# Optimization experiments

Hardware: AMD Instinct MI355X
Metric: run time of the kernel (lower is better)

The kernel has to match this reference:

```python
import jax, jax.numpy as jnp
import numpy as np

B, N, D, H = 8, 1024, 512, 512  # batch, nodes/graph, input dim, hidden/output dim
NEG_SLOPE = 0.2


def _gatv2_layer(x, src, dst, Wl, bl, Wr, br, a, bias, nseg):
    """PyG GATv2Conv (heads=1, add_self_loops=False, eval mode -> no dropout).
    message j->i: alpha_ij = softmax_i( a . leaky_relu(xl[j] + xr[i]) ); out[i] = sum_j alpha_ij * xl[j] + bias
    """
    xl = x @ Wl + bl              # [nseg, H] source transform
    xr = x @ Wr + br              # [nseg, H] target transform
    e = jax.nn.leaky_relu(xl[src] + xr[dst], NEG_SLOPE) @ a  # [E] raw scores
    m = jax.lax.stop_gradient(jax.ops.segment_max(e, dst, num_segments=nseg))
    ex = jnp.exp(e - m[dst])
    s = jax.ops.segment_sum(ex, dst, num_segments=nseg)
    alpha = ex / s[dst]                                       # segment softmax over incoming edges
    out = jax.ops.segment_sum(alpha[:, None] * xl[src], dst, num_segments=nseg)
    return out + bias


def setup_inputs() -> dict:
    key = jax.random.key(0)
    rng = np.random.RandomState(0)
    # random per-graph adjacency, avg degree ~16; block-diagonal edge extraction
    adj_np = (rng.rand(B, N, N) < (16.0 / N))
    srcs, dsts = [], []
    for b in range(B):  # matches torch.nonzero(big_adj).t(): row=src, col=dst
        r, c = np.nonzero(adj_np[b])
        srcs.append(r + b * N)
        dsts.append(c + b * N)
    edge_index = jnp.asarray(np.stack([np.concatenate(srcs), np.concatenate(dsts)]).astype(np.int32))

    ks = jax.random.split(key, 32)
    def lin(k, fi, fo):
        return (jax.random.normal(k, (fi, fo), jnp.float32) / np.sqrt(fi)).astype(jnp.float32)
    inp = {
        "batch_graph": jax.random.normal(ks[0], (B, N, D), jnp.float32),
        "adj": jnp.asarray(adj_np.astype(np.float32)),
        "edge_index": edge_index,
    }
    dims = [(D, H), (H, H), (H, H)]
    for i, (fi, fo) in enumerate(dims, start=1):
        k = jax.random.split(ks[i], 6)
        inp[f"Wl{i}"] = lin(k[0], fi, fo)
        inp[f"bl{i}"] = jnp.zeros((fo,), jnp.float32)
        inp[f"Wr{i}"] = lin(k[1], fi, fo)
        inp[f"br{i}"] = jnp.zeros((fo,), jnp.float32)
        inp[f"a{i}"] = (jax.random.normal(k[2], (fo,), jnp.float32) / np.sqrt(fo)).astype(jnp.float32)
        inp[f"bias{i}"] = jnp.zeros((fo,), jnp.float32)
    return inp


def reference(batch_graph, adj, edge_index,
              Wl1, bl1, Wr1, br1, a1, bias1,
              Wl2, bl2, Wr2, br2, a2, bias2,
              Wl3, bl3, Wr3, br3, a3, bias3):
    b, n, d = batch_graph.shape
    nseg = b * n
    x = batch_graph.reshape(nseg, d)
    src, dst = edge_index[0], edge_index[1]
    x = _gatv2_layer(x, src, dst, Wl1, bl1, Wr1, br1, a1, bias1, nseg)  # graph_norm = Identity
    x = _gatv2_layer(x, src, dst, Wl2, bl2, Wr2, br2, a2, bias2, nseg)
    x = _gatv2_layer(x, src, dst, Wl3, bl3, Wr3, br3, a3, bias3, nseg)
    return x.reshape(b, n, -1)
```

## Files before the change

### kernel.cpp

```cpp
#include <hip/hip_runtime.h>
#include <math.h>

#define MTOT 8192
#define HD   512

typedef __attribute__((ext_vector_type(8))) short bf16x8;
typedef __attribute__((ext_vector_type(4))) float floatx4;

__device__ inline unsigned short f2bf(float f) {
    unsigned int u = __float_as_uint(f);
    unsigned int r = (u + 0x7FFFu + ((u >> 16) & 1u)) >> 16;
    return (unsigned short)r;
}
__device__ inline float bf2f(unsigned short h) {
    return __uint_as_float(((unsigned int)h) << 16);
}


__global__ void count_deg(const int* __restrict__ dst, int* __restrict__ deg, int E) {
    int i = blockIdx.x * 256 + threadIdx.x;
    if (i < E) atomicAdd(&deg[dst[i]], 1);
}

__global__ __launch_bounds__(1024) void scan_offsets(const int* __restrict__ deg,
                                                     int* __restrict__ offs,
                                                     int* __restrict__ cursor) {
    __shared__ int part[1024];
    int tid = threadIdx.x;
    int base = tid * 8;
    int v[8]; int s = 0;
    #pragma unroll
    for (int i = 0; i < 8; ++i) { v[i] = deg[base + i]; s += v[i]; }
    part[tid] = s;
    __syncthreads();
    for (int off = 1; off < 1024; off <<= 1) {
        int t = (tid >= off) ? part[tid - off] : 0;
        __syncthreads();
        part[tid] += t;
        __syncthreads();
    }
    int run = (tid == 0) ? 0 : part[tid - 1];
    #pragma unroll
    for (int i = 0; i < 8; ++i) {
        offs[base + i] = run;
        cursor[base + i] = run;
        run += v[i];
    }
    if (tid == 1023) offs[MTOT] = run;
}

__global__ void scatter_edges(const int* __restrict__ src, const int* __restrict__ dst,
                              int* __restrict__ cursor, int* __restrict__ csr_src, int E) {
    int i = blockIdx.x * 256 + threadIdx.x;
    if (i < E) {
        int p = atomicAdd(&cursor[dst[i]], 1);
        csr_src[p] = src[i];
    }
}


__global__ __launch_bounds__(256) void prep_convert(
    const float* __restrict__ W0, const float* __restrict__ W1,
    const float* __restrict__ W2, const float* __restrict__ W3,
    const float* __restrict__ W4, const float* __restrict__ W5,
    unsigned short* __restrict__ wtbase,
    const float* __restrict__ X,
    unsigned short* __restrict__ Ahi, unsigned short* __restrict__ Alo,
    int* __restrict__ deg)
{
    int z = blockIdx.z;
    if (z == 7) {
        if (blockIdx.x == 0 && blockIdx.y == 0)
            for (int i = threadIdx.x; i < MTOT; i += 256) deg[i] = 0;
        return;
    }
    if (z == 6) {
        int bid = blockIdx.x * 16 + blockIdx.y;
        int t0 = bid * 256 + threadIdx.x;
        #pragma unroll
        for (int it = 0; it < 16; ++it) {
            int i = (t0 + it * 65536) * 4;
            float4 vv = *(const float4*)(X + i);
            ushort4 h, l;
            h.x = f2bf(vv.x); l.x = f2bf(vv.x - bf2f(h.x));
            h.y = f2bf(vv.y); l.y = f2bf(vv.y - bf2f(h.y));
            h.z = f2bf(vv.z); l.z = f2bf(vv.z - bf2f(h.z));
            h.w = f2bf(vv.w); l.w = f2bf(vv.w - bf2f(h.w));
            *(ushort4*)(Ahi + i) = h;
            *(ushort4*)(Alo + i) = l;
        }
        return;
    }
    const float* W = (z == 0) ? W0 : (z == 1) ? W1 : (z == 2) ? W2
                   : (z == 3) ? W3 : (z == 4) ? W4 : W5;
    int L = z >> 1, lr = z & 1;
    const size_t SZ = (size_t)HD * HD;
    unsigned short* Whi = wtbase + (L * 4 + lr * 2) * SZ;
    unsigned short* Wlo = Whi + SZ;

    __shared__ float t[32][33];
    int bx = blockIdx.x * 32;
    int by = blockIdx.y * 32;
    int tx = threadIdx.x & 31, ty = threadIdx.x >> 5;
    for (int i = ty; i < 32; i += 8)
        t[i][tx] = W[(size_t)(by + i) * HD + bx + tx];
    __syncthreads();
    for (int i = ty; i < 32; i += 8) {
        float vv = t[tx][i];
        unsigned short h = f2bf(vv);
        unsigned short l = f2bf(vv - bf2f(h));
        Whi[(size_t)(bx + i) * HD + by + tx] = h;
        Wlo[(size_t)(bx + i) * HD + by + tx] = l;
    }
}


__global__ __launch_bounds__(256) void gemm_mfma_dual(
    const unsigned short* __restrict__ Ahi, const unsigned short* __restrict__ Alo,
    const unsigned short* __restrict__ Bhi_l, const unsigned short* __restrict__ Blo_l,
    const unsigned short* __restrict__ Bhi_r, const unsigned short* __restrict__ Blo_r,
    const float* __restrict__ bias_l, const float* __restrict__ bias_r,
    float* __restrict__ Cl, float* __restrict__ Cr)
{
    const unsigned short* Bhi = blockIdx.z ? Bhi_r : Bhi_l;
    const unsigned short* Blo = blockIdx.z ? Blo_r : Blo_l;
    const float* bias         = blockIdx.z ? bias_r : bias_l;
    float* C                  = blockIdx.z ? Cr : Cl;

    __shared__ __align__(16) unsigned short lds[4 * 128 * 32];

    int tid = threadIdx.x;
    int wave = tid >> 6, lane = tid & 63;
    int bm = blockIdx.y * 128, bn = blockIdx.x * 128;

    const unsigned short* gsrc[4] = {Ahi, Alo, Bhi, Blo};
    int rowbase[4] = {bm, bm, bn, bn};

    const unsigned short* gbase =
        gsrc[wave] + (size_t)(rowbase[wave] + (lane >> 2)) * 512 + (lane & 3) * 8;

    floatx4 acc[4][4] = {};

    int wm = wave & 1, wn = wave >> 1;
    int lr = lane & 15, lq = lane >> 4;

    for (int k0 = 0; k0 < 512; k0 += 32) {
        const unsigned short* g = gbase + k0;
        #pragma unroll
        for (int rg = 0; rg < 8; ++rg) {
            __builtin_amdgcn_global_load_lds(
                (const __attribute__((address_space(1))) unsigned int*)(g + (size_t)rg * 16 * 512),
                (__attribute__((address_space(3))) unsigned int*)(&lds[wave * 4096 + rg * 512]),
                16, 0, 0);
        }
        __syncthreads();

        bf16x8 ah[4], al[4], bh[4], bl_[4];
        #pragma unroll
        for (int i = 0; i < 4; ++i) {
            int mrow = wm * 64 + i * 16 + lr;
            ah[i]  = *(const bf16x8*)&lds[0 * 4096 + mrow * 32 + lq * 8];
            al[i]  = *(const bf16x8*)&lds[1 * 4096 + mrow * 32 + lq * 8];
            int nrow = wn * 64 + i * 16 + lr;
            bh[i]  = *(const bf16x8*)&lds[2 * 4096 + nrow * 32 + lq * 8];
            bl_[i] = *(const bf16x8*)&lds[3 * 4096 + nrow * 32 + lq * 8];
        }
        #pragma unroll
        for (int i = 0; i < 4; ++i)
            #pragma unroll
            for (int j = 0; j < 4; ++j) {
                acc[i][j] = __builtin_amdgcn_mfma_f32_16x16x32_bf16(ah[i], bh[j],  acc[i][j], 0, 0, 0);
                acc[i][j] = __builtin_amdgcn_mfma_f32_16x16x32_bf16(ah[i], bl_[j], acc[i][j], 0, 0, 0);
                acc[i][j] = __builtin_amdgcn_mfma_f32_16x16x32_bf16(al[i], bh[j],  acc[i][j], 0, 0, 0);
            }
        __syncthreads();
    }

    #pragma unroll
    for (int j = 0; j < 4; ++j) {
        int n = bn + wn * 64 + j * 16 + lr;
        float bv = bias[n];
        #pragma unroll
        for (int i = 0; i < 4; ++i) {
            int mbase = bm + wm * 64 + i * 16 + lq * 4;
            #pragma unroll
            for (int r = 0; r < 4; ++r)
                C[(size_t)(mbase + r) * 512 + n] = acc[i][j][r] + bv;
        }
    }
}


__global__ __launch_bounds__(512) void gat_fused3(
    const float* __restrict__ xl, const float* __restrict__ xr,
    const float* __restrict__ avec, const float* __restrict__ bias,
    const int* __restrict__ offs, const int* __restrict__ csr_src,
    float* __restrict__ out, unsigned short* __restrict__ Ohi,
    unsigned short* __restrict__ Olo, int write_fp32)
{
    __shared__ float xr_sh[4][512];
    __shared__ float sc_sh[4][128];
    __shared__ int   idx_sh[4][128];
    __shared__ float inv_sh[4];

    int gid = blockIdx.x;
    int nbase = ((gid & 7) << 10) + ((gid >> 3) << 2);
    int tid = threadIdx.x;
    int wv = tid >> 6, lane = tid & 63;

    int o0 = offs[nbase], o1 = offs[nbase + 1], o2 = offs[nbase + 2];
    int o3 = offs[nbase + 3], o4 = offs[nbase + 4];

    {
        int row = tid >> 7, col = tid & 127;
        *(float4*)&xr_sh[row][col * 4] =
            *(const float4*)(xr + (size_t)(nbase + row) * HD + col * 4);
    }
    if (wv < 4) {
        int nb = (wv == 0) ? o0 : (wv == 1) ? o1 : (wv == 2) ? o2 : o3;
        int ne = (wv == 0) ? o1 : (wv == 1) ? o2 : (wv == 2) ? o3 : o4;
        int dg = ne - nb; if (dg > 128) dg = 128;
        for (int i = lane; i < dg; i += 64) idx_sh[wv][i] = csr_src[nb + i];
    }
    __syncthreads();

    {
        int sub = lane >> 4, flane = lane & 15;
        float4 av[8];
        #pragma unroll
        for (int i = 0; i < 8; ++i)
            av[i] = *(const float4*)(avec + i * 64 + flane * 4);

        for (int p0 = o0 + wv * 4; p0 < o4; p0 += 32) {
            int p = p0 + sub;
            bool valid = p < o4;
            int pc = valid ? p : o0;
            int nid = (pc >= o1) + (pc >= o2) + (pc >= o3);
            int nb = (nid == 0) ? o0 : (nid == 1) ? o1 : (nid == 2) ? o2 : o3;
            int local = pc - nb;
            valid = valid && (local < 128);
            int j = idx_sh[nid][valid ? local : 0];
            const float* xls = xl + (size_t)j * HD;
            float pe0 = 0.f, pe1 = 0.f;
            #pragma unroll
            for (int i = 0; i < 8; ++i) {
                float4 xv = *(const float4*)(xls + i * 64 + flane * 4);
                float4 rv = *(const float4*)&xr_sh[nid][i * 64 + flane * 4];
                float t;
                t = xv.x + rv.x; pe0 = fmaf(av[i].x, t, pe0); pe1 = fmaf(av[i].x, fabsf(t), pe1);
                t = xv.y + rv.y; pe0 = fmaf(av[i].y, t, pe0); pe1 = fmaf(av[i].y, fabsf(t), pe1);
                t = xv.z + rv.z; pe0 = fmaf(av[i].z, t, pe0); pe1 = fmaf(av[i].z, fabsf(t), pe1);
                t = xv.w + rv.w; pe0 = fmaf(av[i].w, t, pe0); pe1 = fmaf(av[i].w, fabsf(t), pe1);
            }
            float pe = fmaf(0.6f, pe0, 0.4f * pe1);
            pe += __shfl_xor(pe, 1, 64);
            pe += __shfl_xor(pe, 2, 64);
            pe += __shfl_xor(pe, 4, 64);
            pe += __shfl_xor(pe, 8, 64);
            if (valid && flane == 0) sc_sh[nid][local] = pe;
        }
    }
    __syncthreads();

    if (wv < 4) {
        int nb = (wv == 0) ? o0 : (wv == 1) ? o1 : (wv == 2) ? o2 : o3;
        int ne = (wv == 0) ? o1 : (wv == 1) ? o2 : (wv == 2) ? o3 : o4;
        int dg = ne - nb; if (dg > 128) dg = 128;
        float s0v = (lane < dg) ? sc_sh[wv][lane] : -1e30f;
        float s1v = (lane + 64 < dg) ? sc_sh[wv][lane + 64] : -1e30f;
        float m = fmaxf(s0v, s1v);
        #pragma unroll
        for (int off = 32; off; off >>= 1) m = fmaxf(m, __shfl_xor(m, off, 64));
        float e0 = (lane < dg) ? __expf(s0v - m) : 0.f;
        float e1 = (lane + 64 < dg) ? __expf(s1v - m) : 0.f;
        if (lane < dg) sc_sh[wv][lane] = e0;
        if (lane + 64 < dg) sc_sh[wv][lane + 64] = e1;
        float s = e0 + e1;
        #pragma unroll
        for (int off = 32; off; off >>= 1) s += __shfl_xor(s, off, 64);
        if (lane == 0) inv_sh[wv] = (s > 0.f) ? 1.f / s : 0.f;
    }
    __syncthreads();

    int nid = wv & 3, half = wv >> 2;
    int node = nbase + nid;
    int nb = (nid == 0) ? o0 : (nid == 1) ? o1 : (nid == 2) ? o2 : o3;
    int ne = (nid == 0) ? o1 : (nid == 1) ? o2 : (nid == 2) ? o3 : o4;
    int dg = ne - nb; if (dg > 128) dg = 128;
    int hb = half * 256 + lane * 4;

    float4 acc = {0.f, 0.f, 0.f, 0.f};
    int p = 0;
    for (; p + 8 <= dg; p += 8) {
        float w[8]; const float* q[8];
        #pragma unroll
        for (int u = 0; u < 8; ++u) {
            w[u] = sc_sh[nid][p + u];
            q[u] = xl + (size_t)idx_sh[nid][p + u] * HD + hb;
        }
        float4 x[8];
        #pragma unroll
        for (int u = 0; u < 8; ++u) x[u] = *(const float4*)q[u];
        #pragma unroll
        for (int u = 0; u < 8; ++u) {
            acc.x += w[u] * x[u].x; acc.y += w[u] * x[u].y;
            acc.z += w[u] * x[u].z; acc.w += w[u] * x[u].w;
        }
    }
    for (; p < dg; ++p) {
        float w = sc_sh[nid][p];
        const float* q = xl + (size_t)idx_sh[nid][p] * HD + hb;
        float4 x = *(const float4*)q;
        acc.x += w * x.x; acc.y += w * x.y; acc.z += w * x.z; acc.w += w * x.w;
    }

    float inv = inv_sh[nid];
    float4 bv = *(const float4*)(bias + hb);
    float4 o = {acc.x * inv + bv.x, acc.y * inv + bv.y,
                acc.z * inv + bv.z, acc.w * inv + bv.w};

    if (write_fp32) {
        *(float4*)(out + (size_t)node * HD + hb) = o;
    } else {
        size_t rb = (size_t)node * HD + hb;
        ushort4 h, lo;
        h.x = f2bf(o.x); lo.x = f2bf(o.x - bf2f(h.x));
        h.y = f2bf(o.y); lo.y = f2bf(o.y - bf2f(h.y));
        h.z = f2bf(o.z); lo.z = f2bf(o.z - bf2f(h.z));
        h.w = f2bf(o.w); lo.w = f2bf(o.w - bf2f(h.w));
        *(ushort4*)(Ohi + rb) = h;
        *(ushort4*)(Olo + rb) = lo;
    }
}


extern "C" void kernel_launch(void* const* d_in, const int* in_sizes, int n_in,
                              void* d_out, int out_size, void* d_ws, size_t ws_size,
                              hipStream_t stream) {
    const float* x0 = (const float*)d_in[0];
    const int* eidx = (const int*)d_in[2];
    int E = in_sizes[2] / 2;
    const int* esrc = eidx;
    const int* edst = eidx + E;

    const float* Wl[3] = {(const float*)d_in[3],  (const float*)d_in[9],  (const float*)d_in[15]};
    const float* bl[3] = {(const float*)d_in[4],  (const float*)d_in[10], (const float*)d_in[16]};
    const float* Wr[3] = {(const float*)d_in[5],  (const float*)d_in[11], (const float*)d_in[17]};
    const float* br[3] = {(const float*)d_in[6],  (const float*)d_in[12], (const float*)d_in[18]};
    const float* av[3] = {(const float*)d_in[7],  (const float*)d_in[13], (const float*)d_in[19]};
    const float* bs[3] = {(const float*)d_in[8],  (const float*)d_in[14], (const float*)d_in[20]};

    char* w = (char*)d_ws;
    unsigned short* Ahi = (unsigned short*)w; w += (size_t)MTOT * HD * 2;
    unsigned short* Alo = (unsigned short*)w; w += (size_t)MTOT * HD * 2;
    unsigned short* wtbase = (unsigned short*)w; w += 12 * (size_t)HD * HD * 2;
    float* xl = (float*)w; w += (size_t)MTOT * HD * 4;
    float* xr = (float*)w; w += (size_t)MTOT * HD * 4;
    int* deg    = (int*)w;
    int* offs   = deg + MTOT;
    int* cursor = offs + MTOT + 8;
    int* csr    = cursor + MTOT;
    const size_t SZ = (size_t)HD * HD;

    prep_convert<<<dim3(16, 16, 8), 256, 0, stream>>>(
        Wl[0], Wr[0], Wl[1], Wr[1], Wl[2], Wr[2], wtbase, x0, Ahi, Alo, deg);
    count_deg<<<(E + 255) / 256, 256, 0, stream>>>(edst, deg, E);
    scan_offsets<<<1, 1024, 0, stream>>>(deg, offs, cursor);
    scatter_edges<<<(E + 255) / 256, 256, 0, stream>>>(esrc, edst, cursor, csr, E);

    dim3 ggrid(HD / 128, MTOT / 128, 2);
    for (int L = 0; L < 3; ++L) {
        gemm_mfma_dual<<<ggrid, 256, 0, stream>>>(Ahi, Alo,
            wtbase + (L * 4 + 0) * SZ, wtbase + (L * 4 + 1) * SZ,
            wtbase + (L * 4 + 2) * SZ, wtbase + (L * 4 + 3) * SZ,
            bl[L], br[L], xl, xr);
        int last = (L == 2);
        gat_fused3<<<MTOT / 4, 512, 0, stream>>>(xl, xr, av[L], bs[L], offs, csr,
                                                 last ? (float*)d_out : nullptr,
                                                 last ? nullptr : Ahi,
                                                 last ? nullptr : Alo,
                                                 last);
    }
}
```

Baseline: 336.1 us.

## Fold degree counting and prefix scan into prep and first GEMM launches

Removes the standalone count_deg and scan_offsets kernels. Degree counting now runs in the z==7 slice of prep_convert after a memset, and the CSR offset scan runs in an extra z==2 slice of the first dual GEMM. This cuts kernel launches and serial gaps in the CSR build, and scatter_edges now runs between the first GEMM and the first attention kernel. The trade-off is an extra memset launch and a 256-thread scan running alongside the GEMM blocks, plus a mostly idle z==2 grid slice in layer one.

```diff
diff --git a/kernel.cpp b/kernel.cpp
--- a/kernel.cpp
+++ b/kernel.cpp
@@ -17,37 +17,6 @@
 }
 
 
-__global__ void count_deg(const int* __restrict__ dst, int* __restrict__ deg, int E) {
-    int i = blockIdx.x * 256 + threadIdx.x;
-    if (i < E) atomicAdd(&deg[dst[i]], 1);
-}
-
-__global__ __launch_bounds__(1024) void scan_offsets(const int* __restrict__ deg,
-                                                     int* __restrict__ offs,
-                                                     int* __restrict__ cursor) {
-    __shared__ int part[1024];
-    int tid = threadIdx.x;
-    int base = tid * 8;
-    int v[8]; int s = 0;
-    #pragma unroll
-    for (int i = 0; i < 8; ++i) { v[i] = deg[base + i]; s += v[i]; }
-    part[tid] = s;
-    __syncthreads();
-    for (int off = 1; off < 1024; off <<= 1) {
-        int t = (tid >= off) ? part[tid - off] : 0;
-        __syncthreads();
-        part[tid] += t;
-        __syncthreads();
-    }
-    int run = (tid == 0) ? 0 : part[tid - 1];
-    #pragma unroll
-    for (int i = 0; i < 8; ++i) {
-        offs[base + i] = run;
-        cursor[base + i] = run;
-        run += v[i];
-    }
-    if (tid == 1023) offs[MTOT] = run;
-}
 
 __global__ void scatter_edges(const int* __restrict__ src, const int* __restrict__ dst,
                               int* __restrict__ cursor, int* __restrict__ csr_src, int E) {
@@ -66,12 +35,12 @@
     unsigned short* __restrict__ wtbase,
     const float* __restrict__ X,
     unsigned short* __restrict__ Ahi, unsigned short* __restrict__ Alo,
-    int* __restrict__ deg)
+    const int* __restrict__ edst, int E, int* __restrict__ deg)
 {
     int z = blockIdx.z;
     if (z == 7) {
-        if (blockIdx.x == 0 && blockIdx.y == 0)
-            for (int i = threadIdx.x; i < MTOT; i += 256) deg[i] = 0;
+        int t0 = (blockIdx.x * 16 + blockIdx.y) * 256 + threadIdx.x;
+        for (int i = t0; i < E; i += 65536) atomicAdd(&deg[edst[i]], 1);
         return;
     }
     if (z == 6) {
@@ -120,8 +89,38 @@
     const unsigned short* __restrict__ Bhi_l, const unsigned short* __restrict__ Blo_l,
     const unsigned short* __restrict__ Bhi_r, const unsigned short* __restrict__ Blo_r,
     const float* __restrict__ bias_l, const float* __restrict__ bias_r,
-    float* __restrict__ Cl, float* __restrict__ Cr)
+    float* __restrict__ Cl, float* __restrict__ Cr,
+    int do_scan, const int* __restrict__ deg,
+    int* __restrict__ offs, int* __restrict__ cursor)
 {
+    if (blockIdx.z == 2) {
+        if (do_scan && blockIdx.x == 0 && blockIdx.y == 0) {
+            __shared__ int part[256];
+            int tid = threadIdx.x;
+            int base = tid * 32;
+            int v[32]; int s = 0;
+            #pragma unroll
+            for (int i = 0; i < 32; ++i) { v[i] = deg[base + i]; s += v[i]; }
+            part[tid] = s;
+            __syncthreads();
+            for (int off = 1; off < 256; off <<= 1) {
+                int t = (tid >= off) ? part[tid - off] : 0;
+                __syncthreads();
+                part[tid] += t;
+                __syncthreads();
+            }
+            int run = tid ? part[tid - 1] : 0;
+            #pragma unroll
+            for (int i = 0; i < 32; ++i) {
+                offs[base + i] = run;
+                cursor[base + i] = run;
+                run += v[i];
+            }
+            if (tid == 255) offs[MTOT] = run;
+        }
+        return;
+    }
+
     const unsigned short* Bhi = blockIdx.z ? Bhi_r : Bhi_l;
     const unsigned short* Blo = blockIdx.z ? Blo_r : Blo_l;
     const float* bias         = blockIdx.z ? bias_r : bias_l;
@@ -362,18 +361,22 @@
     int* csr    = cursor + MTOT;
     const size_t SZ = (size_t)HD * HD;
 
+    hipMemsetAsync(deg, 0, MTOT * sizeof(int), stream);
+
     prep_convert<<<dim3(16, 16, 8), 256, 0, stream>>>(
-        Wl[0], Wr[0], Wl[1], Wr[1], Wl[2], Wr[2], wtbase, x0, Ahi, Alo, deg);
-    count_deg<<<(E + 255) / 256, 256, 0, stream>>>(edst, deg, E);
-    scan_offsets<<<1, 1024, 0, stream>>>(deg, offs, cursor);
-    scatter_edges<<<(E + 255) / 256, 256, 0, stream>>>(esrc, edst, cursor, csr, E);
-
-    dim3 ggrid(HD / 128, MTOT / 128, 2);
+        Wl[0], Wr[0], Wl[1], Wr[1], Wl[2], Wr[2], wtbase, x0, Ahi, Alo,
+        edst, E, deg);
+
     for (int L = 0; L < 3; ++L) {
+        int first = (L == 0);
+        dim3 ggrid(HD / 128, MTOT / 128, first ? 3 : 2);
         gemm_mfma_dual<<<ggrid, 256, 0, stream>>>(Ahi, Alo,
             wtbase + (L * 4 + 0) * SZ, wtbase + (L * 4 + 1) * SZ,
             wtbase + (L * 4 + 2) * SZ, wtbase + (L * 4 + 3) * SZ,
-            bl[L], br[L], xl, xr);
+            bl[L], br[L], xl, xr,
+            first, deg, offs, cursor);
+        if (first)
+            scatter_edges<<<(E + 255) / 256, 256, 0, stream>>>(esrc, edst, cursor, csr, E);
         int last = (L == 2);
         gat_fused3<<<MTOT / 4, 512, 0, stream>>>(xl, xr, av[L], bs[L], offs, csr,
                                                  last ? (float*)d_out : nullptr,
```

New measurement: 337.3 us. About the same (+0.4%).
